# Kernel tuning notes

Hardware: AMD Instinct MI355X
Metric: run time of the kernel (lower is better)

Reference implementation:

```python
import jax, jax.numpy as jnp
import numpy as np

N, E, E_LG = 20000, 320000, 600000
F_NODE, F_EDGE, HID, OUT = 256, 64, 256, 40


def _seg_softmax(e, idx, n):
    m = jax.ops.segment_max(e, idx, num_segments=n)
    ex = jnp.exp(e - m[idx])
    s = jax.ops.segment_sum(ex, idx, num_segments=n)
    return ex / (s[idx] + 1e-16)


def _gat(xf, edge_index, W, a_s, a_d, b, n):
    # PyG-style single-head GATConv with self-loops
    h = xf @ W                                   # [n, HID]
    loops = jnp.arange(n, dtype=edge_index.dtype)
    src = jnp.concatenate([edge_index[0], loops])
    dst = jnp.concatenate([edge_index[1], loops])
    e = jax.nn.leaky_relu((h @ a_s)[src] + (h @ a_d)[dst], 0.2)
    alpha = _seg_softmax(e, dst, n)
    return jax.ops.segment_sum(alpha[:, None] * h[src], dst, num_segments=n) + b


def _sage(xf, src, dst, Wr, Wn, b, n):
    # mean-aggregation SAGEConv with root weight
    deg = jnp.clip(jax.ops.segment_sum(jnp.ones(src.shape, xf.dtype), dst, num_segments=n), 1.0)
    mean = jax.ops.segment_sum(xf[src], dst, num_segments=n) / deg[:, None]
    return xf @ Wr + mean @ Wn + b


def setup_inputs() -> dict:
    key = jax.random.key(0)
    ks = jax.random.split(key, 40)
    g = lambda i, shape, fan: jax.random.normal(ks[i], shape, jnp.float32) * np.float32(np.sqrt(2.0 / fan))
    inp = {
        'x': jax.random.normal(ks[0], (N, F_NODE), jnp.float32),
        'et': jax.random.normal(ks[1], (E, F_EDGE), jnp.float32),
        'H': jax.random.randint(ks[2], (2, E), 0, N, jnp.int32),
        'raw_edge_index': jax.random.randint(ks[3], (2, E), 0, N, jnp.int32),
        'lg_edge_index': jax.random.randint(ks[4], (2, E_LG), 0, E, jnp.int32),
        # EdgeGCNV2: GATConv + EdgeToNodeConv + Linear
        'W_gat': g(5, (F_EDGE, HID), F_EDGE), 'a_src': g(6, (HID,), HID), 'a_dst': g(7, (HID,), HID),
        'b_gat': jnp.zeros((HID,), jnp.float32),
        'W_etn': g(8, (HID, HID), HID), 'W_eg': g(9, (HID, HID), HID),
        # edge_aggr SAGE: num_layers-1 = 2 layers
        'Wr_e1': g(10, (HID, HID), HID), 'Wn_e1': g(11, (HID, HID), HID), 'b_e1': jnp.zeros((HID,), jnp.float32),
        'Wr_e2': g(12, (HID, HID), HID), 'Wn_e2': g(13, (HID, HID), HID), 'b_e2': jnp.zeros((HID,), jnp.float32),
        # attr_node SAGE: num_layers = 3 layers
        'Wr_n1': g(14, (F_NODE, HID), F_NODE), 'Wn_n1': g(15, (F_NODE, HID), F_NODE), 'b_n1': jnp.zeros((HID,), jnp.float32),
        'Wr_n2': g(16, (HID, HID), HID), 'Wn_n2': g(17, (HID, HID), HID), 'b_n2': jnp.zeros((HID,), jnp.float32),
        'Wr_n3': g(18, (HID, HID), HID), 'Wn_n3': g(19, (HID, HID), HID), 'b_n3': jnp.zeros((HID,), jnp.float32),
        # MixAttention
        'Wq': g(20, (HID, HID), HID), 'Wk': g(21, (HID, HID), HID), 'Wv': g(22, (HID, HID), HID),
        # final linear (glorot, no bias)
        'W_out': g(23, (HID, OUT), HID),
    }
    return inp


def reference(x, et, H, raw_edge_index, lg_edge_index,
              W_gat, a_src, a_dst, b_gat, W_etn, W_eg,
              Wr_e1, Wn_e1, b_e1, Wr_e2, Wn_e2, b_e2,
              Wr_n1, Wn_n1, b_n1, Wr_n2, Wn_n2, b_n2, Wr_n3, Wn_n3, b_n3,
              Wq, Wk, Wv, W_out):
    src, dst = raw_edge_index[0], raw_edge_index[1]

    # ---- EdgeGCNV2: GAT over line graph, then edge->node incidence aggregation ----
    gat_out = _gat(et, lg_edge_index, W_gat, a_src, a_dst, b_gat, E)   # [E, HID]
    he = gat_out @ W_etn
    acc = (jax.ops.segment_sum(he, H[0], num_segments=N)
           + jax.ops.segment_sum(he, H[1], num_segments=N))            # [N, HID]
    ones_e = jnp.ones((E,), he.dtype)
    deg = (jax.ops.segment_sum(ones_e, H[0], num_segments=N)
           + jax.ops.segment_sum(ones_e, H[1], num_segments=N))
    etn = acc / jnp.clip(deg, 1.0)[:, None]
    edge_repr = jax.nn.leaky_relu(etn, 0.2) @ W_eg                     # [N, HID]

    # ---- edge_aggr SAGE (2 layers, relu between) ----
    h = jax.nn.relu(_sage(edge_repr, src, dst, Wr_e1, Wn_e1, b_e1, N))
    aggr_edge = _sage(h, src, dst, Wr_e2, Wn_e2, b_e2, N)

    # ---- attr_node SAGE (3 layers) ----
    h = jax.nn.relu(_sage(x, src, dst, Wr_n1, Wn_n1, b_n1, N))
    h = jax.nn.relu(_sage(h, src, dst, Wr_n2, Wn_n2, b_n2, N))
    node_repr = _sage(h, src, dst, Wr_n3, Wn_n3, b_n3, N)

    # ---- MixAttention: node queries attend over neighbor edge-derived keys/values ----
    q, k, v = node_repr @ Wq, aggr_edge @ Wk, aggr_edge @ Wv
    sc = jnp.sum(q[dst] * k[src], axis=-1) * np.float32(1.0 / np.sqrt(HID))
    alpha = _seg_softmax(sc, dst, N)
    mixed = node_repr + jax.ops.segment_sum(alpha[:, None] * v[src], dst, num_segments=N)

    logits = mixed @ W_out
    return jax.nn.log_softmax(logits, axis=1)
```

## Files before the change

kernel.cpp:

```cpp
#include <hip/hip_runtime.h>
#include <math.h>

#define NN   20000
#define EE   320000
#define ELG  600000
#define FE   64
#define HD   256
#define FOUT 40
#define LOG2E 1.44269504f
#define NTOTC (NN + EE + NN)
#define NIDX  (EE + ELG + 2 * EE)
#define RD_RANGE  ((NN + 7) / 8)
#define RLG_RANGE ((EE + 7) / 8)
#define PBLK 256

typedef __attribute__((ext_vector_type(8))) short bf16x8;
typedef __attribute__((ext_vector_type(4))) float f32x4;

__device__ __forceinline__ float leaky02(float x) { return x > 0.f ? x : 0.2f * x; }

__device__ __forceinline__ unsigned short bf16rne(float f) {
    unsigned int u = __float_as_uint(f);
    u = (u + 0x7FFFu + ((u >> 16) & 1u)) >> 16;
    return (unsigned short)u;
}
__device__ __forceinline__ float bflo(unsigned int u) { return __uint_as_float(u << 16); }
__device__ __forceinline__ float bfhi(unsigned int u) { return __uint_as_float(u & 0xffff0000u); }
__device__ __forceinline__ unsigned int bfpack(float a, float b) {
    return (unsigned int)bf16rne(a) | ((unsigned int)bf16rne(b) << 16);
}

__global__ void zero_i32(int* __restrict__ p, int n) {
    int i = blockIdx.x * 256 + threadIdx.x;
    if (i < n) p[i] = 0;
}
__global__ void conv_bf16(const float* __restrict__ in, unsigned int* __restrict__ out, int n2) {
    int i = blockIdx.x * 256 + threadIdx.x;
    if (i < n2) { float2 v = ((const float2*)in)[i]; out[i] = bfpack(v.x, v.y); }
}

__global__ __launch_bounds__(256)
void count_ranged(const int* __restrict__ dstN, const int* __restrict__ lgd,
                  const int* __restrict__ Hm, int* __restrict__ cntAll) {
    int r = blockIdx.x & 7;
    int blk = blockIdx.x >> 3;
    const int stride = PBLK * 256;
    for (int i = blk * 256 + threadIdx.x; i < NIDX; i += stride) {
        if (i < EE) {
            int key = dstN[i];
            if (key / RD_RANGE == r) atomicAdd(&cntAll[key], 1);
        } else if (i < EE + ELG) {
            int key = lgd[i - EE];
            if (key / RLG_RANGE == r) atomicAdd(&cntAll[NN + key], 1);
        } else {
            int key = Hm[i - EE - ELG];
            if (key / RD_RANGE == r) atomicAdd(&cntAll[NN + EE + key], 1);
        }
    }
}

__global__ void scan_pass1(const int* __restrict__ in, int* __restrict__ bsum, int n) {
    __shared__ int sm[256];
    int base = blockIdx.x * 1024, t = threadIdx.x;
    int s = 0;
#pragma unroll
    for (int j = 0; j < 4; ++j) { int i = base + t * 4 + j; s += (i < n) ? in[i] : 0; }
    sm[t] = s; __syncthreads();
    for (int o = 128; o > 0; o >>= 1) { if (t < o) sm[t] += sm[t + o]; __syncthreads(); }
    if (t == 0) bsum[blockIdx.x] = sm[0];
}
__global__ void scan_pass2(int* __restrict__ bsum, int nb) {
    __shared__ int sm[1024];
    int t = threadIdx.x;
    for (int i = t; i < nb; i += 256) sm[i] = bsum[i];
    __syncthreads();
    if (t == 0) { int run = 0; for (int i = 0; i < nb; ++i) { int v = sm[i]; sm[i] = run; run += v; } }
    __syncthreads();
    for (int i = t; i < nb; i += 256) bsum[i] = sm[i];
}
__global__ void scan_pass3(const int* __restrict__ in, const int* __restrict__ boff,
                           int* __restrict__ out, int n) {
    __shared__ int tsum[256];
    int base = blockIdx.x * 1024, t = threadIdx.x;
    int v[4];
#pragma unroll
    for (int j = 0; j < 4; ++j) { int i = base + t * 4 + j; v[j] = (i < n) ? in[i] : 0; }
    int loc = v[0] + v[1] + v[2] + v[3];
    tsum[t] = loc; __syncthreads();
    for (int o = 1; o < 256; o <<= 1) {
        int x = (t >= o) ? tsum[t - o] : 0;
        __syncthreads();
        tsum[t] += x;
        __syncthreads();
    }
    int off = boff[blockIdx.x] + (tsum[t] - loc);
    int run = 0;
#pragma unroll
    for (int j = 0; j < 4; ++j) { int i = base + t * 4 + j; if (i < n) out[i] = off + run; run += v[j]; }
}

__global__ void rebase_all(const int* __restrict__ scanAll,
                           int* __restrict__ rowptrD, int* __restrict__ cursD,
                           int* __restrict__ rowptrLG, int* __restrict__ cursLG,
                           int* __restrict__ rowptrH, int* __restrict__ cursH) {
    int i = blockIdx.x * 256 + threadIdx.x;
    if (i == 0) { rowptrD[NN] = EE; rowptrLG[EE] = ELG; rowptrH[NN] = 2 * EE; }
    if (i >= NTOTC) return;
    if (i < NN) { int v = scanAll[i]; rowptrD[i] = v; cursD[i] = v; }
    else if (i < NN + EE) { int v = scanAll[i] - EE; rowptrLG[i - NN] = v; cursLG[i - NN] = v; }
    else { int v = scanAll[i] - (EE + ELG); rowptrH[i - NN - EE] = v; cursH[i - NN - EE] = v; }
}

__global__ __launch_bounds__(256)
void place_ranged(const int* __restrict__ srcN, const int* __restrict__ dstN,
                  const int* __restrict__ lgs, const int* __restrict__ lgd,
                  const int* __restrict__ Hm,
                  int* __restrict__ cursD, int* __restrict__ cursLG, int* __restrict__ cursH,
                  int* __restrict__ adjS, int* __restrict__ adjLG, int* __restrict__ adjH) {
    int r = blockIdx.x & 7;
    int blk = blockIdx.x >> 3;
    const int stride = PBLK * 256;
    for (int i = blk * 256 + threadIdx.x; i < NIDX; i += stride) {
        if (i < EE) {
            int key = dstN[i];
            if (key / RD_RANGE == r) {
                int pos = atomicAdd(&cursD[key], 1);
                adjS[pos] = srcN[i];
            }
        } else if (i < EE + ELG) {
            int j = i - EE;
            int key = lgd[j];
            if (key / RLG_RANGE == r) {
                int pos = atomicAdd(&cursLG[key], 1);
                adjLG[pos] = lgs[j];
            }
        } else {
            int j = i - EE - ELG;
            int key = Hm[j];
            if (key / RD_RANGE == r) {
                int pos = atomicAdd(&cursH[key], 1);
                adjH[pos] = (j < EE) ? j : j - EE;
            }
        }
    }
}

struct Ptr14 { const float* p[14]; };
__global__ void wtrans14(Ptr14 srcs, unsigned short* __restrict__ dst) {
    int m = blockIdx.x >> 6;
    int tile = blockIdx.x & 63;
    const float* src = srcs.p[m];
    unsigned short* out = dst + (size_t)m * 65536;
    int kb = (tile >> 3) * 32, nb = (tile & 7) * 32;
    __shared__ float sm[32][33];
    int t = threadIdx.x;
#pragma unroll
    for (int i = 0; i < 4; ++i) {
        int e = t + i * 256; int r = e >> 5, c = e & 31;
        sm[r][c] = src[(kb + r) * 256 + nb + c];
    }
    __syncthreads();
#pragma unroll
    for (int i = 0; i < 4; ++i) {
        int e = t + i * 256; int nr = e >> 5, kc = e & 31;
        out[(size_t)(nb + nr) * 256 + kb + kc] = bf16rne(sm[kc][nr]);
    }
}
__global__ void wtrans_one(const float* __restrict__ src, unsigned short* __restrict__ dst,
                           int K, int N) {
    int tilesN = N >> 5;
    int kb = (blockIdx.x / tilesN) * 32, nb = (blockIdx.x % tilesN) * 32;
    __shared__ float sm[32][33];
    int t = threadIdx.x;
#pragma unroll
    for (int i = 0; i < 4; ++i) {
        int e = t + i * 256; int r = e >> 5, c = e & 31;
        sm[r][c] = src[(kb + r) * N + nb + c];
    }
    __syncthreads();
#pragma unroll
    for (int i = 0; i < 4; ++i) {
        int e = t + i * 256; int nr = e >> 5, kc = e & 31;
        dst[(size_t)(nb + nr) * K + kb + kc] = bf16rne(sm[kc][nr]);
    }
}

__global__ __launch_bounds__(256)
void gemm_bf16(const unsigned short* __restrict__ A1, const unsigned short* __restrict__ A2,
               const unsigned short* __restrict__ W1, const unsigned short* __restrict__ W2,
               const float* __restrict__ bias, const float* __restrict__ degmask,
               unsigned short* __restrict__ C, int M, int K1, int flags) {
    __shared__ unsigned short As[128][40];
    __shared__ unsigned short Bs[64][40];
    int tid = threadIdx.x;
    int w = tid >> 6, l = tid & 63;
    int wr = w >> 1, wc = w & 1;
    int brow = blockIdx.y * 128, bcol = blockIdx.x * 64;
    int Ktot = K1 + (A2 ? 256 : 0);
    f32x4 acc[4][2] = {};
    for (int k0 = 0; k0 < Ktot; k0 += 32) {
        const unsigned short* Ap; const unsigned short* Wp; int kk, Klen;
        if (k0 < K1) { Ap = A1; Wp = W1; kk = k0; Klen = K1; }
        else         { Ap = A2; Wp = W2; kk = k0 - K1; Klen = 256; }
#pragma unroll
        for (int i = 0; i < 4; ++i) {
            int q = tid + i * 256;
            int r = q >> 3, kb = (q & 7) * 4;
            int gr = brow + r;
            ushort4 u;
            if (gr < M) u = *(const ushort4*)(Ap + (size_t)gr * Klen + kk + kb);
            else { u.x = 0; u.y = 0; u.z = 0; u.w = 0; }
            *(ushort4*)(&As[r][kb]) = u;
        }
#pragma unroll
        for (int i = 0; i < 2; ++i) {
            int q = tid + i * 256;
            int n = q >> 3, kb = (q & 7) * 4;
            *(ushort4*)(&Bs[n][kb]) = *(const ushort4*)(Wp + (size_t)(bcol + n) * Klen + kk + kb);
        }
        __syncthreads();
        bf16x8 af[4], bfr[2];
#pragma unroll
        for (int fr = 0; fr < 4; ++fr)
            af[fr] = *(const bf16x8*)(&As[wr * 64 + fr * 16 + (l & 15)][(l >> 4) * 8]);
#pragma unroll
        for (int fc = 0; fc < 2; ++fc)
            bfr[fc] = *(const bf16x8*)(&Bs[wc * 32 + fc * 16 + (l & 15)][(l >> 4) * 8]);
#pragma unroll
        for (int fr = 0; fr < 4; ++fr)
#pragma unroll
            for (int fc = 0; fc < 2; ++fc)
                acc[fr][fc] = __builtin_amdgcn_mfma_f32_16x16x32_bf16(af[fr], bfr[fc], acc[fr][fc], 0, 0, 0);
        __syncthreads();
    }
#pragma unroll
    for (int fr = 0; fr < 4; ++fr) {
#pragma unroll
        for (int fc = 0; fc < 2; ++fc) {
            int col = bcol + wc * 32 + fc * 16 + (l & 15);
#pragma unroll
            for (int i = 0; i < 4; ++i) {
                int row = brow + wr * 64 + fr * 16 + (l >> 4) * 4 + i;
                if (row >= M) continue;
                float v = acc[fr][fc][i];
                if (bias) v += bias[col];
                if (flags & 1) v = fmaxf(v, 0.f);
                if (flags & 4) { v = (degmask[row] > 0.f) ? v : 0.f; v = leaky02(v); }
                C[(size_t)row * 256 + col] = bf16rne(v);
            }
        }
    }
}

__global__ __launch_bounds__(256)
void gemm_bf16_tri(const unsigned short* __restrict__ A0, const unsigned short* __restrict__ W0,
                   unsigned short* __restrict__ C0,
                   const unsigned short* __restrict__ A1, const unsigned short* __restrict__ W1,
                   unsigned short* __restrict__ C1,
                   const unsigned short* __restrict__ A2, const unsigned short* __restrict__ W2,
                   unsigned short* __restrict__ C2, int M) {
    __shared__ unsigned short As[128][40];
    __shared__ unsigned short Bs[64][40];
    int sel = blockIdx.x >> 2;
    const unsigned short* A = (sel == 0) ? A0 : (sel == 1) ? A1 : A2;
    const unsigned short* W = (sel == 0) ? W0 : (sel == 1) ? W1 : W2;
    unsigned short* C = (sel == 0) ? C0 : (sel == 1) ? C1 : C2;
    int tid = threadIdx.x;
    int w = tid >> 6, l = tid & 63;
    int wr = w >> 1, wc = w & 1;
    int brow = blockIdx.y * 128, bcol = (blockIdx.x & 3) * 64;
    f32x4 acc[4][2] = {};
    for (int k0 = 0; k0 < 256; k0 += 32) {
#pragma unroll
        for (int i = 0; i < 4; ++i) {
            int q = tid + i * 256;
            int r = q >> 3, kb = (q & 7) * 4;
            int gr = brow + r;
            ushort4 u;
            if (gr < M) u = *(const ushort4*)(A + (size_t)gr * 256 + k0 + kb);
            else { u.x = 0; u.y = 0; u.z = 0; u.w = 0; }
            *(ushort4*)(&As[r][kb]) = u;
        }
#pragma unroll
        for (int i = 0; i < 2; ++i) {
            int q = tid + i * 256;
            int n = q >> 3, kb = (q & 7) * 4;
            *(ushort4*)(&Bs[n][kb]) = *(const ushort4*)(W + (size_t)(bcol + n) * 256 + k0 + kb);
        }
        __syncthreads();
        bf16x8 af[4], bfr[2];
#pragma unroll
        for (int fr = 0; fr < 4; ++fr)
            af[fr] = *(const bf16x8*)(&As[wr * 64 + fr * 16 + (l & 15)][(l >> 4) * 8]);
#pragma unroll
        for (int fc = 0; fc < 2; ++fc)
            bfr[fc] = *(const bf16x8*)(&Bs[wc * 32 + fc * 16 + (l & 15)][(l >> 4) * 8]);
#pragma unroll
        for (int fr = 0; fr < 4; ++fr)
#pragma unroll
            for (int fc = 0; fc < 2; ++fc)
                acc[fr][fc] = __builtin_amdgcn_mfma_f32_16x16x32_bf16(af[fr], bfr[fc], acc[fr][fc], 0, 0, 0);
        __syncthreads();
    }
#pragma unroll
    for (int fr = 0; fr < 4; ++fr) {
#pragma unroll
        for (int fc = 0; fc < 2; ++fc) {
            int col = bcol + wc * 32 + fc * 16 + (l & 15);
#pragma unroll
            for (int i = 0; i < 4; ++i) {
                int row = brow + wr * 64 + fr * 16 + (l >> 4) * 4 + i;
                if (row >= M) continue;
                C[(size_t)row * 256 + col] = bf16rne(acc[fr][fc][i]);
            }
        }
    }
}

__global__ __launch_bounds__(256)
void gemm_f32(const float* __restrict__ A, const float* __restrict__ B,
              float* __restrict__ C, int M, int N, int K) {
    const int BM = 64, BN = 64, BK = 16;
    __shared__ float As[BK][BM + 1];
    __shared__ float Bs[BK][BN + 1];
    int tid = threadIdx.x;
    int tr = tid >> 4, tc = tid & 15;
    int brow = blockIdx.y * BM, bcol = blockIdx.x * BN;
    float acc[4][4] = {{0.f}};
    for (int k0 = 0; k0 < K; k0 += BK) {
#pragma unroll
        for (int i = 0; i < 4; ++i) {
            int e = tid + i * 256;
            int r = e >> 4, c = e & 15;
            int gr = brow + r, gc = k0 + c;
            As[c][r] = (gr < M && gc < K) ? A[(long)gr * K + gc] : 0.f;
        }
#pragma unroll
        for (int i = 0; i < 4; ++i) {
            int e = tid + i * 256;
            int r = e >> 6, c = e & 63;
            int gr = k0 + r, gc = bcol + c;
            Bs[r][c] = (gr < K && gc < N) ? B[(long)gr * N + gc] : 0.f;
        }
        __syncthreads();
#pragma unroll
        for (int k = 0; k < BK; ++k) {
            float ra[4], rb[4];
#pragma unroll
            for (int i = 0; i < 4; ++i) ra[i] = As[k][tr * 4 + i];
#pragma unroll
            for (int j = 0; j < 4; ++j) rb[j] = Bs[k][tc * 4 + j];
#pragma unroll
            for (int i = 0; i < 4; ++i)
#pragma unroll
                for (int j = 0; j < 4; ++j) acc[i][j] += ra[i] * rb[j];
        }
        __syncthreads();
    }
#pragma unroll
    for (int i = 0; i < 4; ++i) {
        int gr = brow + tr * 4 + i;
        if (gr >= M) continue;
#pragma unroll
        for (int j = 0; j < 4; ++j) {
            int gc = bcol + tc * 4 + j;
            if (gc < N) C[(long)gr * N + gc] = acc[i][j];
        }
    }
}

__global__ __launch_bounds__(256)
void gemm_out_lsm(const float* __restrict__ A, const float* __restrict__ B,
                  float* __restrict__ out, int M) {
    const int BK = 16;
    __shared__ float As[BK][65];
    __shared__ float Bs[BK][65];
    __shared__ float tile[64][41];
    __shared__ float lsb[64];
    int tid = threadIdx.x;
    int tr = tid >> 4, tc = tid & 15;
    int brow = blockIdx.y * 64;
    float acc[4][4] = {{0.f}};
    for (int k0 = 0; k0 < 256; k0 += BK) {
#pragma unroll
        for (int i = 0; i < 4; ++i) {
            int e = tid + i * 256;
            int r = e >> 4, c = e & 15;
            int gr = brow + r;
            As[c][r] = (gr < M) ? A[(long)gr * 256 + k0 + c] : 0.f;
        }
#pragma unroll
        for (int i = 0; i < 4; ++i) {
            int e = tid + i * 256;
            int r = e >> 6, c = e & 63;
            Bs[r][c] = (c < FOUT) ? B[(long)(k0 + r) * FOUT + c] : 0.f;
        }
        __syncthreads();
#pragma unroll
        for (int k = 0; k < BK; ++k) {
            float ra[4], rb[4];
#pragma unroll
            for (int i = 0; i < 4; ++i) ra[i] = As[k][tr * 4 + i];
#pragma unroll
            for (int j = 0; j < 4; ++j) rb[j] = Bs[k][tc * 4 + j];
#pragma unroll
            for (int i = 0; i < 4; ++i)
#pragma unroll
                for (int j = 0; j < 4; ++j) acc[i][j] += ra[i] * rb[j];
        }
        __syncthreads();
    }
#pragma unroll
    for (int i = 0; i < 4; ++i)
#pragma unroll
        for (int j = 0; j < 4; ++j) {
            int gc = tc * 4 + j;
            if (gc < FOUT) tile[tr * 4 + i][gc] = acc[i][j];
        }
    __syncthreads();
    if (tid < 64) {
        int gr = brow + tid;
        float mx = -INFINITY;
        if (gr < M) {
            for (int c = 0; c < FOUT; ++c) mx = fmaxf(mx, tile[tid][c]);
            float s = 0.f;
            for (int c = 0; c < FOUT; ++c) s += __expf(tile[tid][c] - mx);
            lsb[tid] = mx + logf(s);
        }
    }
    __syncthreads();
#pragma unroll
    for (int i = 0; i < 4; ++i) {
        int r = tr * 4 + i;
        int gr = brow + r;
        if (gr >= M) continue;
#pragma unroll
        for (int j = 0; j < 4; ++j) {
            int gc = tc * 4 + j;
            if (gc < FOUT) out[(long)gr * FOUT + gc] = tile[r][gc] - lsb[r];
        }
    }
}

__global__ void gat_prep(const float* __restrict__ W, const float* __restrict__ as_,
                         const float* __restrict__ ad_, const float* __restrict__ b_gat,
                         const float* __restrict__ W_etn,
                         float* __restrict__ asv, float* __restrict__ adv, float* __restrict__ b2) {
    int t = threadIdx.x;
    if (blockIdx.x == FE) {
        float s = 0.f;
        for (int i = 0; i < HD; ++i) s += b_gat[i] * W_etn[i * HD + t];
        b2[t] = s;
        return;
    }
    __shared__ float sm[256];
    int i = blockIdx.x;
    float w = W[i * HD + t];
    sm[t] = w * as_[t];
    __syncthreads();
    for (int o = 128; o > 0; o >>= 1) { if (t < o) sm[t] += sm[t + o]; __syncthreads(); }
    if (t == 0) asv[i] = sm[0];
    __syncthreads();
    sm[t] = w * ad_[t];
    __syncthreads();
    for (int o = 128; o > 0; o >>= 1) { if (t < o) sm[t] += sm[t + o]; __syncthreads(); }
    if (t == 0) adv[i] = sm[0];
}

__global__ void edge_scores_conv(const float* __restrict__ et, const float* __restrict__ asv,
                                 const float* __restrict__ adv, float* __restrict__ es,
                                 float* __restrict__ ed, unsigned short* __restrict__ et_bf) {
    int e = blockIdx.x * 4 + (threadIdx.x >> 6);
    int l = threadIdx.x & 63;
    float x = et[(long)e * FE + l];
    et_bf[(long)e * FE + l] = bf16rne(x);
    float vs = x * asv[l];
    float vd = x * adv[l];
    for (int o = 32; o > 0; o >>= 1) { vs += __shfl_down(vs, o); vd += __shfl_down(vd, o); }
    if (l == 0) { es[e] = vs; ed[e] = vd; }
}

__global__ void seg_alpha(const int* __restrict__ rowptr, const int* __restrict__ adj,
                          const float* __restrict__ es, const float* __restrict__ ed,
                          float* __restrict__ alphaS, float* __restrict__ alphaL) {
    int d = blockIdx.x * 256 + threadIdx.x;
    if (d >= EE) return;
    int b = rowptr[d], e_ = rowptr[d + 1];
    float edd = ed[d];
    float selfsc = leaky02(es[d] + edd);
    float m = selfsc;
    for (int i = b; i < e_; ++i) m = fmaxf(m, leaky02(es[adj[i]] + edd));
    float s = __expf(selfsc - m);
    for (int i = b; i < e_; ++i) s += __expf(leaky02(es[adj[i]] + edd) - m);
    float inv = 1.f / (s + 1e-16f);
    alphaS[d] = __expf(selfsc - m) * inv;
    for (int i = b; i < e_; ++i) alphaL[i] = __expf(leaky02(es[adj[i]] + edd) - m) * inv;
}

__global__ void gat_gather3(const int* __restrict__ rowptr, const int* __restrict__ adj,
                            const float* __restrict__ alphaS, const float* __restrict__ alphaL,
                            const unsigned short* __restrict__ et_bf,
                            unsigned short* __restrict__ agg_et) {
    int d = blockIdx.x * 32 + (threadIdx.x >> 3);
    int hl = threadIdx.x & 7;
    if (d >= EE) return;
    int b = rowptr[d], e_ = rowptr[d + 1];
    const uint4* etu = (const uint4*)et_bf;
    int i = b;
    float aln = 0.f; uint4 un;
    if (i < e_) { aln = alphaL[i]; un = etu[(size_t)adj[i] * 8 + hl]; }
    float al = alphaS[d];
    uint4 u = etu[(size_t)d * 8 + hl];
    float a0 = al * bflo(u.x), a1 = al * bfhi(u.x), a2 = al * bflo(u.y), a3 = al * bfhi(u.y);
    float a4 = al * bflo(u.z), a5 = al * bfhi(u.z), a6 = al * bflo(u.w), a7 = al * bfhi(u.w);
    while (i < e_) {
        float alc = aln; uint4 uc = un;
        int in = i + 1;
        if (in < e_) { aln = alphaL[in]; un = etu[(size_t)adj[in] * 8 + hl]; }
        a0 += alc * bflo(uc.x); a1 += alc * bfhi(uc.x); a2 += alc * bflo(uc.y); a3 += alc * bfhi(uc.y);
        a4 += alc * bflo(uc.z); a5 += alc * bfhi(uc.z); a6 += alc * bflo(uc.w); a7 += alc * bfhi(uc.w);
        i = in;
    }
    uint4 o;
    o.x = bfpack(a0, a1); o.y = bfpack(a2, a3); o.z = bfpack(a4, a5); o.w = bfpack(a6, a7);
    ((uint4*)agg_et)[(size_t)d * 8 + hl] = o;
}

__global__ void etn_gather3(const int* __restrict__ rowptr, const int* __restrict__ adj,
                            const unsigned short* __restrict__ agg_et,
                            unsigned short* __restrict__ agg2, float* __restrict__ degE) {
    int n = blockIdx.x * 32 + (threadIdx.x >> 3);
    int hl = threadIdx.x & 7;
    if (n >= NN) return;
    int b = rowptr[n], e_ = rowptr[n + 1];
    const uint4* au = (const uint4*)agg_et;
    int i = b;
    uint4 un;
    if (i < e_) un = au[(size_t)adj[i] * 8 + hl];
    float a0 = 0.f, a1 = 0.f, a2 = 0.f, a3 = 0.f, a4 = 0.f, a5 = 0.f, a6 = 0.f, a7 = 0.f;
    while (i < e_) {
        uint4 uc = un;
        int in = i + 1;
        if (in < e_) un = au[(size_t)adj[in] * 8 + hl];
        a0 += bflo(uc.x); a1 += bfhi(uc.x); a2 += bflo(uc.y); a3 += bfhi(uc.y);
        a4 += bflo(uc.z); a5 += bfhi(uc.z); a6 += bflo(uc.w); a7 += bfhi(uc.w);
        i = in;
    }
    float deg = (float)(e_ - b);
    float inv = 1.f / fmaxf(deg, 1.f);
    uint4 o;
    o.x = bfpack(a0 * inv, a1 * inv); o.y = bfpack(a2 * inv, a3 * inv);
    o.z = bfpack(a4 * inv, a5 * inv); o.w = bfpack(a6 * inv, a7 * inv);
    ((uint4*)agg2)[(size_t)n * 8 + hl] = o;
    if (hl == 0) degE[n] = deg;
}

__global__ void sage_gather2(const unsigned short* __restrict__ X, const int* __restrict__ rowptr,
                             const int* __restrict__ adjS, unsigned short* __restrict__ mean) {
    int base = (blockIdx.x * 4 + (threadIdx.x >> 6)) * 2;
    int lane = threadIdx.x & 63;
    int half = lane >> 5, hl = lane & 31;
    int n = base + half;
    if (n >= NN) return;
    int b = rowptr[n], e_ = rowptr[n + 1];
    const uint4* Xu = (const uint4*)X;
    int i = b;
    uint4 un;
    if (i < e_) un = Xu[(size_t)adjS[i] * 32 + hl];
    float a0 = 0.f, a1 = 0.f, a2 = 0.f, a3 = 0.f, a4 = 0.f, a5 = 0.f, a6 = 0.f, a7 = 0.f;
    while (i < e_) {
        uint4 uc = un;
        int in = i + 1;
        if (in < e_) un = Xu[(size_t)adjS[in] * 32 + hl];
        a0 += bflo(uc.x); a1 += bfhi(uc.x); a2 += bflo(uc.y); a3 += bfhi(uc.y);
        a4 += bflo(uc.z); a5 += bfhi(uc.z); a6 += bflo(uc.w); a7 += bfhi(uc.w);
        i = in;
    }
    float inv = 1.f / fmaxf((float)(e_ - b), 1.f);
    uint4 o;
    o.x = bfpack(a0 * inv, a1 * inv); o.y = bfpack(a2 * inv, a3 * inv);
    o.z = bfpack(a4 * inv, a5 * inv); o.w = bfpack(a6 * inv, a7 * inv);
    ((uint4*)mean)[(size_t)n * 32 + hl] = o;
}

__global__ void attn_online(const unsigned short* __restrict__ q, const unsigned short* __restrict__ k,
                            const unsigned short* __restrict__ v, const unsigned short* __restrict__ nrep,
                            const int* __restrict__ rowptr, const int* __restrict__ adjS,
                            float* __restrict__ mixed) {
    int n = blockIdx.x * 4 + (threadIdx.x >> 6);
    int lane = threadIdx.x & 63;
    if (n >= NN) return;
    int half = lane >> 5, hl = lane & 31;
    int b = rowptr[n], e_ = rowptr[n + 1];
    const uint4* qu4 = (const uint4*)q;
    const uint4* ku4 = (const uint4*)k;
    const uint4* vu4 = (const uint4*)v;
    const uint4* nu4 = (const uint4*)nrep;
    uint4 nu = nu4[(size_t)n * 32 + hl];
    float nr0 = bflo(nu.x), nr1 = bfhi(nu.x), nr2 = bflo(nu.y), nr3 = bfhi(nu.y);
    float nr4 = bflo(nu.z), nr5 = bfhi(nu.z), nr6 = bflo(nu.w), nr7 = bfhi(nu.w);
    float* mrow = mixed + (size_t)n * HD;
    if (b == e_) {
        if (half == 0) {
            ((float4*)mrow)[2 * hl]     = make_float4(nr0, nr1, nr2, nr3);
            ((float4*)mrow)[2 * hl + 1] = make_float4(nr4, nr5, nr6, nr7);
        }
        return;
    }
    uint4 qv = qu4[(size_t)n * 32 + hl];
    float q0 = bflo(qv.x), q1 = bfhi(qv.x), q2 = bflo(qv.y), q3 = bfhi(qv.y);
    float q4 = bflo(qv.z), q5 = bfhi(qv.z), q6 = bflo(qv.w), q7 = bfhi(qv.w);
    float m = -INFINITY, srun = 0.f;
    float a0 = 0.f, a1 = 0.f, a2 = 0.f, a3 = 0.f, a4 = 0.f, a5 = 0.f, a6 = 0.f, a7 = 0.f;
    int i = b + half;
    uint4 ku, vu;
    if (i < e_) {
        int s0 = adjS[i];
        ku = ku4[(size_t)s0 * 32 + hl];
        vu = vu4[(size_t)s0 * 32 + hl];
    }
    while (i < e_) {
        int in = i + 2;
        uint4 kn, vn;
        if (in < e_) {
            int s1 = adjS[in];
            kn = ku4[(size_t)s1 * 32 + hl];
            vn = vu4[(size_t)s1 * 32 + hl];
        }
        float p = q0 * bflo(ku.x) + q1 * bfhi(ku.x) + q2 * bflo(ku.y) + q3 * bfhi(ku.y)
                + q4 * bflo(ku.z) + q5 * bfhi(ku.z) + q6 * bflo(ku.w) + q7 * bfhi(ku.w);
        p += __shfl_xor(p, 1); p += __shfl_xor(p, 2); p += __shfl_xor(p, 4);
        p += __shfl_xor(p, 8); p += __shfl_xor(p, 16);
        p *= 0.0625f;
        float mn = fmaxf(m, p);
        float scale = exp2f((m - mn) * LOG2E);
        float w = exp2f((p - mn) * LOG2E);
        m = mn;
        srun = srun * scale + w;
        a0 = a0 * scale + w * bflo(vu.x); a1 = a1 * scale + w * bfhi(vu.x);
        a2 = a2 * scale + w * bflo(vu.y); a3 = a3 * scale + w * bfhi(vu.y);
        a4 = a4 * scale + w * bflo(vu.z); a5 = a5 * scale + w * bfhi(vu.z);
        a6 = a6 * scale + w * bflo(vu.w); a7 = a7 * scale + w * bfhi(vu.w);
        i = in; ku = kn; vu = vn;
    }
    float mo = __shfl_xor(m, 32);
    float so = __shfl_xor(srun, 32);
    float mn = fmaxf(m, mo);
    float cs = exp2f((m - mn) * LOG2E);
    float co = exp2f((mo - mn) * LOG2E);
    float st = srun * cs + so * co;
    float inv = 1.f / (st + 1e-16f);
    float o0 = (a0 * cs + __shfl_xor(a0, 32) * co) * inv + nr0;
    float o1 = (a1 * cs + __shfl_xor(a1, 32) * co) * inv + nr1;
    float o2 = (a2 * cs + __shfl_xor(a2, 32) * co) * inv + nr2;
    float o3 = (a3 * cs + __shfl_xor(a3, 32) * co) * inv + nr3;
    float o4 = (a4 * cs + __shfl_xor(a4, 32) * co) * inv + nr4;
    float o5 = (a5 * cs + __shfl_xor(a5, 32) * co) * inv + nr5;
    float o6 = (a6 * cs + __shfl_xor(a6, 32) * co) * inv + nr6;
    float o7 = (a7 * cs + __shfl_xor(a7, 32) * co) * inv + nr7;
    if (half == 0) {
        ((float4*)mrow)[2 * hl]     = make_float4(o0, o1, o2, o3);
        ((float4*)mrow)[2 * hl + 1] = make_float4(o4, o5, o6, o7);
    }
}

extern "C" void kernel_launch(void* const* d_in, const int* in_sizes, int n_in,
                              void* d_out, int out_size, void* d_ws, size_t ws_size,
                              hipStream_t stream) {
    (void)in_sizes; (void)n_in; (void)out_size; (void)ws_size;
    const float* x     = (const float*)d_in[0];
    const float* et    = (const float*)d_in[1];
    const int*   Hm    = (const int*)d_in[2];
    const int*   raw   = (const int*)d_in[3];
    const int*   lg    = (const int*)d_in[4];
    const float* W_gat = (const float*)d_in[5];
    const float* a_src = (const float*)d_in[6];
    const float* a_dst = (const float*)d_in[7];
    const float* b_gat = (const float*)d_in[8];
    const float* W_etn = (const float*)d_in[9];
    const float* W_eg  = (const float*)d_in[10];
    const float* Wr_e1 = (const float*)d_in[11];
    const float* Wn_e1 = (const float*)d_in[12];
    const float* b_e1  = (const float*)d_in[13];
    const float* Wr_e2 = (const float*)d_in[14];
    const float* Wn_e2 = (const float*)d_in[15];
    const float* b_e2  = (const float*)d_in[16];
    const float* Wr_n1 = (const float*)d_in[17];
    const float* Wn_n1 = (const float*)d_in[18];
    const float* b_n1  = (const float*)d_in[19];
    const float* Wr_n2 = (const float*)d_in[20];
    const float* Wn_n2 = (const float*)d_in[21];
    const float* b_n2  = (const float*)d_in[22];
    const float* Wr_n3 = (const float*)d_in[23];
    const float* Wn_n3 = (const float*)d_in[24];
    const float* b_n3  = (const float*)d_in[25];
    const float* Wq    = (const float*)d_in[26];
    const float* Wk    = (const float*)d_in[27];
    const float* Wv    = (const float*)d_in[28];
    const float* W_out = (const float*)d_in[29];

    const int* srcN = raw;
    const int* dstN = raw + EE;
    const int* lgs  = lg;
    const int* lgd  = lg + ELG;

    float* ws = (float*)d_ws;
    size_t off = 0;
    auto alloc = [&](size_t n) { float* p = ws + off; off += (n + 63) & ~(size_t)63; return p; };
    auto allocU = [&](size_t nus) { return (unsigned short*)alloc(nus / 2 + 64); };

    unsigned short* et_bf   = allocU((size_t)EE * FE);
    unsigned short* agg_et  = allocU((size_t)EE * FE);
    float* es     = alloc(EE);
    float* ed     = alloc(EE);
    float* alphaS = alloc(EE);
    float* alphaL = alloc(ELG);
    float* Wcomb  = alloc((size_t)FE * HD);
    float* b2     = alloc(HD);
    float* asv    = alloc(FE);
    float* adv    = alloc(FE);
    unsigned short* agg2_bf = allocU((size_t)NN * FE);
    float* degE   = alloc(NN);
    unsigned short* etnL  = allocU((size_t)NN * HD);
    unsigned short* erep  = allocU((size_t)NN * HD);
    unsigned short* meanb = allocU((size_t)NN * HD);
    unsigned short* t1    = allocU((size_t)NN * HD);
    unsigned short* aggr  = allocU((size_t)NN * HD);
    unsigned short* nrep  = allocU((size_t)NN * HD);
    unsigned short* x_bf  = allocU((size_t)NN * HD);
    float* mixed  = alloc((size_t)NN * HD);
    unsigned short* wtb    = allocU((size_t)14 * 65536);
    unsigned short* wcombt = allocU((size_t)HD * FE);
    int* rowptrD  = (int*)alloc(NN + 64);
    int* cursD    = (int*)alloc(NN);
    int* adjS     = (int*)alloc(EE);
    int* rowptrLG = (int*)alloc(EE + 64);
    int* cursLG   = (int*)alloc(EE);
    int* adjLG    = (int*)alloc(ELG);
    int* rowptrH  = (int*)alloc(NN + 64);
    int* cursH    = (int*)alloc(NN);
    int* adjH     = (int*)alloc(2 * EE);
    int* cntAll   = (int*)alloc(NTOTC + 64);
    int* scanAll  = (int*)alloc(NTOTC + 64);
    int* bsum     = (int*)alloc(1024);
    unsigned short* ta = etnL;
    unsigned short* tb = erep;
    unsigned short* qb = agg_et;
    unsigned short* kb = agg_et + (size_t)NN * HD;
    unsigned short* vb = agg_et + (size_t)2 * NN * HD;
    float* outp = (float*)d_out;

    unsigned short* W_eg_t  = wtb + 0 * 65536;
    unsigned short* Wr_e1_t = wtb + 1 * 65536;
    unsigned short* Wn_e1_t = wtb + 2 * 65536;
    unsigned short* Wr_e2_t = wtb + 3 * 65536;
    unsigned short* Wn_e2_t = wtb + 4 * 65536;
    unsigned short* Wr_n1_t = wtb + 5 * 65536;
    unsigned short* Wn_n1_t = wtb + 6 * 65536;
    unsigned short* Wr_n2_t = wtb + 7 * 65536;
    unsigned short* Wn_n2_t = wtb + 8 * 65536;
    unsigned short* Wr_n3_t = wtb + 9 * 65536;
    unsigned short* Wn_n3_t = wtb + 10 * 65536;
    unsigned short* Wq_t    = wtb + 11 * 65536;
    unsigned short* Wk_t    = wtb + 12 * 65536;
    unsigned short* Wv_t    = wtb + 13 * 65536;

    dim3 gB(4, (NN + 127) / 128);

    Ptr14 p14;
    p14.p[0] = W_eg;  p14.p[1] = Wr_e1; p14.p[2] = Wn_e1; p14.p[3] = Wr_e2;
    p14.p[4] = Wn_e2; p14.p[5] = Wr_n1; p14.p[6] = Wn_n1; p14.p[7] = Wr_n2;
    p14.p[8] = Wn_n2; p14.p[9] = Wr_n3; p14.p[10] = Wn_n3; p14.p[11] = Wq;
    p14.p[12] = Wk;   p14.p[13] = Wv;
    wtrans14<<<14 * 64, 256, 0, stream>>>(p14, wtb);
    conv_bf16<<<(NN * HD / 2 + 255) / 256, 256, 0, stream>>>(x, (unsigned int*)x_bf, NN * HD / 2);

    zero_i32<<<(NTOTC + 255) / 256, 256, 0, stream>>>(cntAll, NTOTC);
    count_ranged<<<8 * PBLK, 256, 0, stream>>>(dstN, lgd, Hm, cntAll);
    {
        int nb = (NTOTC + 1023) / 1024;
        scan_pass1<<<nb, 256, 0, stream>>>(cntAll, bsum, NTOTC);
        scan_pass2<<<1, 256, 0, stream>>>(bsum, nb);
        scan_pass3<<<nb, 256, 0, stream>>>(cntAll, bsum, scanAll, NTOTC);
    }
    rebase_all<<<(NTOTC + 255) / 256, 256, 0, stream>>>(scanAll, rowptrD, cursD,
                                                        rowptrLG, cursLG, rowptrH, cursH);
    place_ranged<<<8 * PBLK, 256, 0, stream>>>(srcN, dstN, lgs, lgd, Hm,
                                               cursD, cursLG, cursH, adjS, adjLG, adjH);

    gemm_f32<<<dim3(4, 1), 256, 0, stream>>>(W_gat, W_etn, Wcomb, FE, HD, HD);
    wtrans_one<<<(FE / 32) * (HD / 32), 256, 0, stream>>>(Wcomb, wcombt, FE, HD);
    gat_prep<<<FE + 1, 256, 0, stream>>>(W_gat, a_src, a_dst, b_gat, W_etn, asv, adv, b2);
    edge_scores_conv<<<EE / 4, 256, 0, stream>>>(et, asv, adv, es, ed, et_bf);
    seg_alpha<<<(EE + 255) / 256, 256, 0, stream>>>(rowptrLG, adjLG, es, ed, alphaS, alphaL);
    gat_gather3<<<EE / 32, 256, 0, stream>>>(rowptrLG, adjLG, alphaS, alphaL, et_bf, agg_et);

    etn_gather3<<<(NN + 31) / 32, 256, 0, stream>>>(rowptrH, adjH, agg_et, agg2_bf, degE);
    gemm_bf16<<<gB, 256, 0, stream>>>(agg2_bf, nullptr, wcombt, nullptr, b2, degE, etnL, NN, FE, 4);
    gemm_bf16<<<gB, 256, 0, stream>>>(etnL, nullptr, W_eg_t, nullptr, nullptr, nullptr, erep, NN, HD, 0);

    sage_gather2<<<(NN + 7) / 8, 256, 0, stream>>>(erep, rowptrD, adjS, meanb);
    gemm_bf16<<<gB, 256, 0, stream>>>(erep, meanb, Wr_e1_t, Wn_e1_t, b_e1, nullptr, t1, NN, HD, 1);
    sage_gather2<<<(NN + 7) / 8, 256, 0, stream>>>(t1, rowptrD, adjS, meanb);
    gemm_bf16<<<gB, 256, 0, stream>>>(t1, meanb, Wr_e2_t, Wn_e2_t, b_e2, nullptr, aggr, NN, HD, 0);

    sage_gather2<<<(NN + 7) / 8, 256, 0, stream>>>(x_bf, rowptrD, adjS, meanb);
    gemm_bf16<<<gB, 256, 0, stream>>>(x_bf, meanb, Wr_n1_t, Wn_n1_t, b_n1, nullptr, ta, NN, HD, 1);
    sage_gather2<<<(NN + 7) / 8, 256, 0, stream>>>(ta, rowptrD, adjS, meanb);
    gemm_bf16<<<gB, 256, 0, stream>>>(ta, meanb, Wr_n2_t, Wn_n2_t, b_n2, nullptr, tb, NN, HD, 1);
    sage_gather2<<<(NN + 7) / 8, 256, 0, stream>>>(tb, rowptrD, adjS, meanb);
    gemm_bf16<<<gB, 256, 0, stream>>>(tb, meanb, Wr_n3_t, Wn_n3_t, b_n3, nullptr, nrep, NN, HD, 0);

    gemm_bf16_tri<<<dim3(12, (NN + 127) / 128), 256, 0, stream>>>(
        nrep, Wq_t, qb, aggr, Wk_t, kb, aggr, Wv_t, vb, NN);
    attn_online<<<(NN + 3) / 4, 256, 0, stream>>>(qb, kb, vb, nrep, rowptrD, adjS, mixed);

    gemm_out_lsm<<<dim3(1, (NN + 63) / 64), 256, 0, stream>>>(mixed, W_out, outp, NN);
}
```

Baseline: 859.6 us.

## Build CSR adjacency with LDS-privatized histograms and cursors per key range

Replaces the global-atomic counting and placement kernels for the three CSR builds with block-per-key-range kernels that keep per-key counts and cursors in shared memory. Each of 48 blocks scans its whole index array and only handles keys in its range. This removes the zeroing kernel and the cursor arrays and turns global atomics into LDS atomics. In exchange only 48 blocks run, and each reads the full edge list, so 8 to 32 blocks redundantly stream the same data with limited parallelism.

```diff
diff --git a/kernel.cpp b/kernel.cpp
--- a/kernel.cpp
+++ b/kernel.cpp
@@ -9,10 +9,12 @@
 #define FOUT 40
 #define LOG2E 1.44269504f
 #define NTOTC (NN + EE + NN)
-#define NIDX  (EE + ELG + 2 * EE)
-#define RD_RANGE  ((NN + 7) / 8)
-#define RLG_RANGE ((EE + 7) / 8)
-#define PBLK 256
+#define DCLS 8
+#define DRNG 2500
+#define LGCLS 32
+#define LGRNG 10000
+#define HCLS 8
+#define HRNG 2500
 
 typedef __attribute__((ext_vector_type(8))) short bf16x8;
 typedef __attribute__((ext_vector_type(4))) float f32x4;
@@ -30,32 +32,47 @@
     return (unsigned int)bf16rne(a) | ((unsigned int)bf16rne(b) << 16);
 }
 
-__global__ void zero_i32(int* __restrict__ p, int n) {
-    int i = blockIdx.x * 256 + threadIdx.x;
-    if (i < n) p[i] = 0;
-}
 __global__ void conv_bf16(const float* __restrict__ in, unsigned int* __restrict__ out, int n2) {
     int i = blockIdx.x * 256 + threadIdx.x;
     if (i < n2) { float2 v = ((const float2*)in)[i]; out[i] = bfpack(v.x, v.y); }
 }
 
 __global__ __launch_bounds__(256)
-void count_ranged(const int* __restrict__ dstN, const int* __restrict__ lgd,
-                  const int* __restrict__ Hm, int* __restrict__ cntAll) {
-    int r = blockIdx.x & 7;
-    int blk = blockIdx.x >> 3;
-    const int stride = PBLK * 256;
-    for (int i = blk * 256 + threadIdx.x; i < NIDX; i += stride) {
-        if (i < EE) {
-            int key = dstN[i];
-            if (key / RD_RANGE == r) atomicAdd(&cntAll[key], 1);
-        } else if (i < EE + ELG) {
-            int key = lgd[i - EE];
-            if (key / RLG_RANGE == r) atomicAdd(&cntAll[NN + key], 1);
-        } else {
-            int key = Hm[i - EE - ELG];
-            if (key / RD_RANGE == r) atomicAdd(&cntAll[NN + EE + key], 1);
-        }
+void count_priv(const int* __restrict__ dstN, const int* __restrict__ lgd,
+                const int* __restrict__ Hm, int* __restrict__ cntAll) {
+    __shared__ int hist[LGRNG];
+    int cb = blockIdx.x;
+    int t = threadIdx.x;
+    if (cb < DCLS) {
+        int base = cb * DRNG;
+        for (int i = t; i < DRNG; i += 256) hist[i] = 0;
+        __syncthreads();
+        for (int i = t; i < EE; i += 256) {
+            unsigned key = (unsigned)(dstN[i] - base);
+            if (key < DRNG) atomicAdd(&hist[key], 1);
+        }
+        __syncthreads();
+        for (int i = t; i < DRNG; i += 256) cntAll[base + i] = hist[i];
+    } else if (cb < DCLS + LGCLS) {
+        int base = (cb - DCLS) * LGRNG;
+        for (int i = t; i < LGRNG; i += 256) hist[i] = 0;
+        __syncthreads();
+        for (int i = t; i < ELG; i += 256) {
+            unsigned key = (unsigned)(lgd[i] - base);
+            if (key < LGRNG) atomicAdd(&hist[key], 1);
+        }
+        __syncthreads();
+        for (int i = t; i < LGRNG; i += 256) cntAll[NN + base + i] = hist[i];
+    } else {
+        int base = (cb - DCLS - LGCLS) * HRNG;
+        for (int i = t; i < HRNG; i += 256) hist[i] = 0;
+        __syncthreads();
+        for (int i = t; i < 2 * EE; i += 256) {
+            unsigned key = (unsigned)(Hm[i] - base);
+            if (key < HRNG) atomicAdd(&hist[key], 1);
+        }
+        __syncthreads();
+        for (int i = t; i < HRNG; i += 256) cntAll[NN + EE + base + i] = hist[i];
     }
 }
 
@@ -100,46 +117,57 @@
 }
 
 __global__ void rebase_all(const int* __restrict__ scanAll,
-                           int* __restrict__ rowptrD, int* __restrict__ cursD,
-                           int* __restrict__ rowptrLG, int* __restrict__ cursLG,
-                           int* __restrict__ rowptrH, int* __restrict__ cursH) {
+                           int* __restrict__ rowptrD, int* __restrict__ rowptrLG,
+                           int* __restrict__ rowptrH) {
     int i = blockIdx.x * 256 + threadIdx.x;
     if (i == 0) { rowptrD[NN] = EE; rowptrLG[EE] = ELG; rowptrH[NN] = 2 * EE; }
     if (i >= NTOTC) return;
-    if (i < NN) { int v = scanAll[i]; rowptrD[i] = v; cursD[i] = v; }
-    else if (i < NN + EE) { int v = scanAll[i] - EE; rowptrLG[i - NN] = v; cursLG[i - NN] = v; }
-    else { int v = scanAll[i] - (EE + ELG); rowptrH[i - NN - EE] = v; cursH[i - NN - EE] = v; }
+    if (i < NN) rowptrD[i] = scanAll[i];
+    else if (i < NN + EE) rowptrLG[i - NN] = scanAll[i] - EE;
+    else rowptrH[i - NN - EE] = scanAll[i] - (EE + ELG);
 }
 
 __global__ __launch_bounds__(256)
-void place_ranged(const int* __restrict__ srcN, const int* __restrict__ dstN,
-                  const int* __restrict__ lgs, const int* __restrict__ lgd,
-                  const int* __restrict__ Hm,
-                  int* __restrict__ cursD, int* __restrict__ cursLG, int* __restrict__ cursH,
-                  int* __restrict__ adjS, int* __restrict__ adjLG, int* __restrict__ adjH) {
-    int r = blockIdx.x & 7;
-    int blk = blockIdx.x >> 3;
-    const int stride = PBLK * 256;
-    for (int i = blk * 256 + threadIdx.x; i < NIDX; i += stride) {
-        if (i < EE) {
-            int key = dstN[i];
-            if (key / RD_RANGE == r) {
-                int pos = atomicAdd(&cursD[key], 1);
+void place_priv(const int* __restrict__ srcN, const int* __restrict__ dstN,
+                const int* __restrict__ lgs, const int* __restrict__ lgd,
+                const int* __restrict__ Hm,
+                const int* __restrict__ rowptrD, const int* __restrict__ rowptrLG,
+                const int* __restrict__ rowptrH,
+                int* __restrict__ adjS, int* __restrict__ adjLG, int* __restrict__ adjH) {
+    __shared__ int cur[LGRNG];
+    int cb = blockIdx.x;
+    int t = threadIdx.x;
+    if (cb < DCLS) {
+        int base = cb * DRNG;
+        for (int i = t; i < DRNG; i += 256) cur[i] = rowptrD[base + i];
+        __syncthreads();
+        for (int i = t; i < EE; i += 256) {
+            unsigned key = (unsigned)(dstN[i] - base);
+            if (key < DRNG) {
+                int pos = atomicAdd(&cur[key], 1);
                 adjS[pos] = srcN[i];
             }
-        } else if (i < EE + ELG) {
-            int j = i - EE;
-            int key = lgd[j];
-            if (key / RLG_RANGE == r) {
-                int pos = atomicAdd(&cursLG[key], 1);
-                adjLG[pos] = lgs[j];
+        }
+    } else if (cb < DCLS + LGCLS) {
+        int base = (cb - DCLS) * LGRNG;
+        for (int i = t; i < LGRNG; i += 256) cur[i] = rowptrLG[base + i];
+        __syncthreads();
+        for (int i = t; i < ELG; i += 256) {
+            unsigned key = (unsigned)(lgd[i] - base);
+            if (key < LGRNG) {
+                int pos = atomicAdd(&cur[key], 1);
+                adjLG[pos] = lgs[i];
             }
-        } else {
-            int j = i - EE - ELG;
-            int key = Hm[j];
-            if (key / RD_RANGE == r) {
-                int pos = atomicAdd(&cursH[key], 1);
-                adjH[pos] = (j < EE) ? j : j - EE;
+        }
+    } else {
+        int base = (cb - DCLS - LGCLS) * HRNG;
+        for (int i = t; i < HRNG; i += 256) cur[i] = rowptrH[base + i];
+        __syncthreads();
+        for (int i = t; i < 2 * EE; i += 256) {
+            unsigned key = (unsigned)(Hm[i] - base);
+            if (key < HRNG) {
+                int pos = atomicAdd(&cur[key], 1);
+                adjH[pos] = (i < EE) ? i : i - EE;
             }
         }
     }
@@ -732,13 +760,10 @@
     unsigned short* wtb    = allocU((size_t)14 * 65536);
     unsigned short* wcombt = allocU((size_t)HD * FE);
     int* rowptrD  = (int*)alloc(NN + 64);
-    int* cursD    = (int*)alloc(NN);
     int* adjS     = (int*)alloc(EE);
     int* rowptrLG = (int*)alloc(EE + 64);
-    int* cursLG   = (int*)alloc(EE);
     int* adjLG    = (int*)alloc(ELG);
     int* rowptrH  = (int*)alloc(NN + 64);
-    int* cursH    = (int*)alloc(NN);
     int* adjH     = (int*)alloc(2 * EE);
     int* cntAll   = (int*)alloc(NTOTC + 64);
     int* scanAll  = (int*)alloc(NTOTC + 64);
@@ -775,18 +800,17 @@
     wtrans14<<<14 * 64, 256, 0, stream>>>(p14, wtb);
     conv_bf16<<<(NN * HD / 2 + 255) / 256, 256, 0, stream>>>(x, (unsigned int*)x_bf, NN * HD / 2);
 
-    zero_i32<<<(NTOTC + 255) / 256, 256, 0, stream>>>(cntAll, NTOTC);
-    count_ranged<<<8 * PBLK, 256, 0, stream>>>(dstN, lgd, Hm, cntAll);
+    count_priv<<<DCLS + LGCLS + HCLS, 256, 0, stream>>>(dstN, lgd, Hm, cntAll);
     {
         int nb = (NTOTC + 1023) / 1024;
         scan_pass1<<<nb, 256, 0, stream>>>(cntAll, bsum, NTOTC);
         scan_pass2<<<1, 256, 0, stream>>>(bsum, nb);
         scan_pass3<<<nb, 256, 0, stream>>>(cntAll, bsum, scanAll, NTOTC);
     }
-    rebase_all<<<(NTOTC + 255) / 256, 256, 0, stream>>>(scanAll, rowptrD, cursD,
-                                                        rowptrLG, cursLG, rowptrH, cursH);
-    place_ranged<<<8 * PBLK, 256, 0, stream>>>(srcN, dstN, lgs, lgd, Hm,
-                                               cursD, cursLG, cursH, adjS, adjLG, adjH);
+    rebase_all<<<(NTOTC + 255) / 256, 256, 0, stream>>>(scanAll, rowptrD, rowptrLG, rowptrH);
+    place_priv<<<DCLS + LGCLS + HCLS, 256, 0, stream>>>(srcN, dstN, lgs, lgd, Hm,
+                                                        rowptrD, rowptrLG, rowptrH,
+                                                        adjS, adjLG, adjH);
 
     gemm_f32<<<dim3(4, 1), 256, 0, stream>>>(W_gat, W_etn, Wcomb, FE, HD, HD);
     wtrans_one<<<(FE / 32) * (HD / 32), 256, 0, stream>>>(Wcomb, wcombt, FE, HD);
```

Result: slower. 2.761 ms (+221.1%).

## Fuse GAT segment softmax into gather using online softmax

Applied to the files above, without the earlier changes.

Merges the separate segment-softmax kernel and the weighted gather kernel into a single kernel. The new kernel computes the attention weights on the fly with a running max and rescaled running sum (online softmax). This removes one launch, the alphaS/alphaL intermediate buffers, and the triple pass over neighbors in seg_alpha. In exchange it adds per-edge exp and rescale arithmetic, and the score loads are now repeated across the 8 lanes that share a node.

```diff
diff --git a/kernel.cpp b/kernel.cpp
--- a/kernel.cpp
+++ b/kernel.cpp
@@ -480,49 +480,44 @@
     if (l == 0) { es[e] = vs; ed[e] = vd; }
 }
 
-__global__ void seg_alpha(const int* __restrict__ rowptr, const int* __restrict__ adj,
-                          const float* __restrict__ es, const float* __restrict__ ed,
-                          float* __restrict__ alphaS, float* __restrict__ alphaL) {
-    int d = blockIdx.x * 256 + threadIdx.x;
-    if (d >= EE) return;
-    int b = rowptr[d], e_ = rowptr[d + 1];
-    float edd = ed[d];
-    float selfsc = leaky02(es[d] + edd);
-    float m = selfsc;
-    for (int i = b; i < e_; ++i) m = fmaxf(m, leaky02(es[adj[i]] + edd));
-    float s = __expf(selfsc - m);
-    for (int i = b; i < e_; ++i) s += __expf(leaky02(es[adj[i]] + edd) - m);
-    float inv = 1.f / (s + 1e-16f);
-    alphaS[d] = __expf(selfsc - m) * inv;
-    for (int i = b; i < e_; ++i) alphaL[i] = __expf(leaky02(es[adj[i]] + edd) - m) * inv;
-}
-
-__global__ void gat_gather3(const int* __restrict__ rowptr, const int* __restrict__ adj,
-                            const float* __restrict__ alphaS, const float* __restrict__ alphaL,
-                            const unsigned short* __restrict__ et_bf,
-                            unsigned short* __restrict__ agg_et) {
+__global__ void gat_fused2(const int* __restrict__ rowptr, const int* __restrict__ adj,
+                           const float* __restrict__ es, const float* __restrict__ ed,
+                           const unsigned short* __restrict__ et_bf,
+                           unsigned short* __restrict__ agg_et) {
     int d = blockIdx.x * 32 + (threadIdx.x >> 3);
     int hl = threadIdx.x & 7;
     if (d >= EE) return;
     int b = rowptr[d], e_ = rowptr[d + 1];
     const uint4* etu = (const uint4*)et_bf;
+    float edd = ed[d];
+    float m = leaky02(es[d] + edd);
+    float srun = 1.f;
+    uint4 u = etu[(size_t)d * 8 + hl];
+    float a0 = bflo(u.x), a1 = bfhi(u.x), a2 = bflo(u.y), a3 = bfhi(u.y);
+    float a4 = bflo(u.z), a5 = bfhi(u.z), a6 = bflo(u.w), a7 = bfhi(u.w);
     int i = b;
-    float aln = 0.f; uint4 un;
-    if (i < e_) { aln = alphaL[i]; un = etu[(size_t)adj[i] * 8 + hl]; }
-    float al = alphaS[d];
-    uint4 u = etu[(size_t)d * 8 + hl];
-    float a0 = al * bflo(u.x), a1 = al * bfhi(u.x), a2 = al * bflo(u.y), a3 = al * bfhi(u.y);
-    float a4 = al * bflo(u.z), a5 = al * bfhi(u.z), a6 = al * bflo(u.w), a7 = al * bfhi(u.w);
+    float esn = 0.f; uint4 un;
+    if (i < e_) { int s0 = adj[i]; esn = es[s0]; un = etu[(size_t)s0 * 8 + hl]; }
     while (i < e_) {
-        float alc = aln; uint4 uc = un;
+        float esc = esn; uint4 uc = un;
         int in = i + 1;
-        if (in < e_) { aln = alphaL[in]; un = etu[(size_t)adj[in] * 8 + hl]; }
-        a0 += alc * bflo(uc.x); a1 += alc * bfhi(uc.x); a2 += alc * bflo(uc.y); a3 += alc * bfhi(uc.y);
-        a4 += alc * bflo(uc.z); a5 += alc * bfhi(uc.z); a6 += alc * bflo(uc.w); a7 += alc * bfhi(uc.w);
+        if (in < e_) { int s1 = adj[in]; esn = es[s1]; un = etu[(size_t)s1 * 8 + hl]; }
+        float p = leaky02(esc + edd);
+        float mn = fmaxf(m, p);
+        float scale = exp2f((m - mn) * LOG2E);
+        float w = exp2f((p - mn) * LOG2E);
+        m = mn;
+        srun = srun * scale + w;
+        a0 = a0 * scale + w * bflo(uc.x); a1 = a1 * scale + w * bfhi(uc.x);
+        a2 = a2 * scale + w * bflo(uc.y); a3 = a3 * scale + w * bfhi(uc.y);
+        a4 = a4 * scale + w * bflo(uc.z); a5 = a5 * scale + w * bfhi(uc.z);
+        a6 = a6 * scale + w * bflo(uc.w); a7 = a7 * scale + w * bfhi(uc.w);
         i = in;
     }
+    float inv = 1.f / (srun + 1e-16f);
     uint4 o;
-    o.x = bfpack(a0, a1); o.y = bfpack(a2, a3); o.z = bfpack(a4, a5); o.w = bfpack(a6, a7);
+    o.x = bfpack(a0 * inv, a1 * inv); o.y = bfpack(a2 * inv, a3 * inv);
+    o.z = bfpack(a4 * inv, a5 * inv); o.w = bfpack(a6 * inv, a7 * inv);
     ((uint4*)agg_et)[(size_t)d * 8 + hl] = o;
 }
 
@@ -713,8 +708,6 @@
     unsigned short* agg_et  = allocU((size_t)EE * FE);
     float* es     = alloc(EE);
     float* ed     = alloc(EE);
-    float* alphaS = alloc(EE);
-    float* alphaL = alloc(ELG);
     float* Wcomb  = alloc((size_t)FE * HD);
     float* b2     = alloc(HD);
     float* asv    = alloc(FE);
@@ -792,8 +785,7 @@
     wtrans_one<<<(FE / 32) * (HD / 32), 256, 0, stream>>>(Wcomb, wcombt, FE, HD);
     gat_prep<<<FE + 1, 256, 0, stream>>>(W_gat, a_src, a_dst, b_gat, W_etn, asv, adv, b2);
     edge_scores_conv<<<EE / 4, 256, 0, stream>>>(et, asv, adv, es, ed, et_bf);
-    seg_alpha<<<(EE + 255) / 256, 256, 0, stream>>>(rowptrLG, adjLG, es, ed, alphaS, alphaL);
-    gat_gather3<<<EE / 32, 256, 0, stream>>>(rowptrLG, adjLG, alphaS, alphaL, et_bf, agg_et);
+    gat_fused2<<<EE / 32, 256, 0, stream>>>(rowptrLG, adjLG, es, ed, et_bf, agg_et);
 
     etn_gather3<<<(NN + 31) / 32, 256, 0, stream>>>(rowptrH, adjH, agg_et, agg2_bf, degE);
     gemm_bf16<<<gB, 256, 0, stream>>>(agg2_bf, nullptr, wcombt, nullptr, b2, degE, etnL, NN, FE, 4);
```

Result: no change. 847.0 us (-1.5%).
